# Optimization experiments

Measured on AMD Instinct MI355X. Metric: run time of the kernel, lower is better.

## Reference

```python
import jax, jax.numpy as jnp
import numpy as np
import math

B, T, C, E, H = 16, 256, 6, 512, 8


def setup_inputs() -> dict:
    key = jax.random.key(0)
    ks = jax.random.split(key, 5)
    std = 0.02
    return {
        "x": jax.random.normal(ks[0], (B, T, C, E), dtype=jnp.float32),
        "Wq": jax.random.normal(ks[1], (E, E), dtype=jnp.float32) * std,
        "bq": jnp.zeros((E,), dtype=jnp.float32),
        "Wk": jax.random.normal(ks[2], (E, E), dtype=jnp.float32) * std,
        "bk": jnp.zeros((E,), dtype=jnp.float32),
        "Wv": jax.random.normal(ks[3], (E, E), dtype=jnp.float32) * std,
        "bv": jnp.zeros((E,), dtype=jnp.float32),
        "Wp": jax.random.normal(ks[4], (E, E), dtype=jnp.float32) * std,
        "bp": jnp.zeros((E,), dtype=jnp.float32),
    }


def reference(x, Wq, bq, Wk, bk, Wv, bv, Wp, bp):
    b, t, c, e = x.shape
    hd = e // H
    # nn.Linear: y = x @ W^T + b, then view(B,T,C,H,hd).transpose(1,3) -> (B,H,C,T,hd)
    def heads(W, bias):
        y = jnp.einsum('btce,fe->btcf', x, W) + bias
        return y.reshape(b, t, c, H, hd).transpose(0, 3, 2, 1, 4)  # B,H,C,T,hd

    q = heads(Wq, bq)
    k = heads(Wk, bk)
    v = heads(Wv, bv)

    scale = 1.0 / math.sqrt(hd)
    att = jnp.einsum('bhctd,bhcsd->bhcts', q, k) * scale  # B,H,C,T,T
    causal = jnp.tril(jnp.ones((t, t), dtype=bool))
    att = jnp.where(causal, att, -jnp.inf)
    att = jax.nn.softmax(att, axis=-1)

    y = jnp.einsum('bhcts,bhcsd->bhctd', att, v)  # B,H,C,T,hd
    # permute(0,3,1,2,4) -> (B,T,H,C,hd), then view(B,T,C,E) (faithful to torch)
    y = y.transpose(0, 3, 1, 2, 4).reshape(b, t, c, e)
    return jnp.einsum('btce,fe->btcf', y, Wp) + bp
```

## Files before the change

kernel.cpp:

```cpp
#include <hip/hip_runtime.h>


typedef unsigned short u16;
typedef short bf16x8 __attribute__((ext_vector_type(8)));
typedef float f32x4 __attribute__((ext_vector_type(4)));
typedef u16 u16x4 __attribute__((ext_vector_type(4)));

#define MFMA16(a, b, c) __builtin_amdgcn_mfma_f32_16x16x32_bf16((a), (b), (c), 0, 0, 0)

__device__ __forceinline__ u16 f2b(float f) {
  union { float f; unsigned u; } v; v.f = f;
  unsigned r = v.u + 0x7fffu + ((v.u >> 16) & 1u);
  return (u16)(r >> 16);
}
__device__ __forceinline__ void gl_lds16(const void* g, void* l) {
  __builtin_amdgcn_global_load_lds(
      (const __attribute__((address_space(1))) void*)g,
      (__attribute__((address_space(3))) void*)l, 16, 0, 0);
}

__global__ void cvt_w(const float* W0, const float* W1, const float* W2,
                      const float* W3, u16* dst) {
  const float* src = (blockIdx.y == 0) ? W0 : (blockIdx.y == 1) ? W1
                   : (blockIdx.y == 2) ? W2 : W3;
  const int idx = (blockIdx.x * 256 + threadIdx.x) * 4;
  f32x4 v = *(const f32x4*)(src + idx);
  u16x4 o; o.x = f2b(v.x); o.y = f2b(v.y); o.z = f2b(v.z); o.w = f2b(v.w);
  *(u16x4*)(dst + (size_t)blockIdx.y * 262144 + idx) = o;
}

__global__ void cvt_x(const float* __restrict__ src, u16* __restrict__ dst) {
  const size_t idx = ((size_t)blockIdx.x * 256 + threadIdx.x) * 4;
  f32x4 v = *(const f32x4*)(src + idx);
  u16x4 o; o.x = f2b(v.x); o.y = f2b(v.y); o.z = f2b(v.z); o.w = f2b(v.w);
  *(u16x4*)(dst + idx) = o;
}

__global__ __launch_bounds__(256, 3) void gemm_bt(
    const u16* __restrict__ A,
    const u16* W0, const u16* W1, const u16* W2,
    const float* bs0, const float* bs1, const float* bs2,
    u16* O0, u16* O1, u16* O2,
    float* OF,
    int qkv_mode)
{
  const int z = blockIdx.z;
  const u16* W    = (z == 0) ? W0 : (z == 1) ? W1 : W2;
  const float* bs = (z == 0) ? bs0 : (z == 1) ? bs1 : bs2;
  u16* O          = (z == 0) ? O0 : (z == 1) ? O1 : O2;

  const int m0 = blockIdx.x * 128;
  const int n0 = blockIdx.y * 128;

  __shared__ u16 As[128 * 32];
  __shared__ u16 Bs[128 * 32];

  const int tid  = threadIdx.x;
  const int lane = tid & 63;
  const int wv   = tid >> 6;
  const int r    = lane & 15;
  const int qd   = lane >> 4;
  const int wm   = (wv & 1) * 64;
  const int wn   = (wv >> 1) * 64;

  f32x4 acc[4][4] = {};

  for (int k0 = 0; k0 < 512; k0 += 32) {
    __syncthreads();
    #pragma unroll
    for (int it = 0; it < 2; ++it) {
      const int flat = (it * 256 + tid) * 16;
      const int row  = flat >> 6;
      const int swc  = (flat >> 4) & 3;
      const int gc   = (swc - (row >> 1)) & 3;
      gl_lds16((const char*)A + (size_t)(m0 + row) * 1024 + k0 * 2 + gc * 16,
               (char*)As + flat);
      gl_lds16((const char*)W + (size_t)(n0 + row) * 1024 + k0 * 2 + gc * 16,
               (char*)Bs + flat);
    }
    __syncthreads();

    bf16x8 af[4], bf[4];
    #pragma unroll
    for (int mt = 0; mt < 4; ++mt) {
      const int row = wm + mt * 16 + r;
      const int sw  = (qd + (row >> 1)) & 3;
      af[mt] = *(const bf16x8*)((const char*)As + row * 64 + sw * 16);
    }
    #pragma unroll
    for (int nt = 0; nt < 4; ++nt) {
      const int row = wn + nt * 16 + r;
      const int sw  = (qd + (row >> 1)) & 3;
      bf[nt] = *(const bf16x8*)((const char*)Bs + row * 64 + sw * 16);
    }
    #pragma unroll
    for (int mt = 0; mt < 4; ++mt)
      #pragma unroll
      for (int nt = 0; nt < 4; ++nt)
        acc[mt][nt] = MFMA16(af[mt], bf[nt], acc[mt][nt]);
  }

  float bv[4];
  #pragma unroll
  for (int nt = 0; nt < 4; ++nt) bv[nt] = bs[n0 + wn + nt * 16 + r];

  if (qkv_mode) {
    #pragma unroll
    for (int mt = 0; mt < 4; ++mt) {
      #pragma unroll
      for (int rr = 0; rr < 4; ++rr) {
        const int m   = m0 + wm + mt * 16 + qd * 4 + rr;
        const int b   = m / 1536;
        const int rem = m - b * 1536;
        const int t   = rem / 6;
        const int c   = rem - t * 6;
        #pragma unroll
        for (int nt = 0; nt < 4; ++nt) {
          const int f = n0 + wn + nt * 16 + r;
          const int h = f >> 6;
          const int d = f & 63;
          const size_t addr = ((((size_t)b * 8 + h) * 6 + c) * 256 + t) * 64 + d;
          O[addr] = f2b(acc[mt][nt][rr] + bv[nt]);
        }
      }
    }
  } else {
    #pragma unroll
    for (int mt = 0; mt < 4; ++mt) {
      #pragma unroll
      for (int rr = 0; rr < 4; ++rr) {
        const int m = m0 + wm + mt * 16 + qd * 4 + rr;
        #pragma unroll
        for (int nt = 0; nt < 4; ++nt) {
          const int f = n0 + wn + nt * 16 + r;
          OF[(size_t)m * 512 + f] = acc[mt][nt][rr] + bv[nt];
        }
      }
    }
  }
}

__global__ __launch_bounds__(512, 2) void attn(
    const u16* __restrict__ q_ws, const u16* __restrict__ k_ws,
    const u16* __restrict__ v_ws, u16* __restrict__ y_ws)
{
  const int blk = blockIdx.x;
  const int b   = blk / 48;
  const int h   = (blk / 6) % 8;
  const int c   = blk % 6;
  const size_t base = (size_t)blk * 256 * 64;

  __shared__ u16 Ks[128 * 72];
  __shared__ u16 Vts[64 * 136];
  __shared__ u16 Ps[8][16 * 72];

  const int tid  = threadIdx.x;
  const int lane = tid & 63;
  const int wv   = tid >> 6;
  const int r    = lane & 15;
  const int qd   = lane >> 4;

  const int tiles[2] = { wv, 15 - wv };

  bf16x8 qf[2][2];
  #pragma unroll
  for (int ti = 0; ti < 2; ++ti)
    #pragma unroll
    for (int kc = 0; kc < 2; ++kc)
      qf[ti][kc] = *(const bf16x8*)(q_ws + base +
                     (size_t)(tiles[ti] * 16 + r) * 64 + kc * 32 + qd * 8);

  f32x4 o_acc[2][4] = {};
  float l_acc[2][4] = {{0.f,0.f,0.f,0.f},{0.f,0.f,0.f,0.f}};

  for (int sc = 0; sc < 2; ++sc) {
    __syncthreads();
    #pragma unroll
    for (int it = 0; it < 2; ++it) {
      const int idx = it * 512 + tid;
      const int row = idx >> 3;
      const int c8  = idx & 7;
      *(bf16x8*)(Ks + row * 72 + c8 * 8) =
          *(const bf16x8*)(k_ws + base + (size_t)(sc * 128 + row) * 64 + c8 * 8);
    }
    {
      const int jl = tid & 127;
      const int d0 = (tid >> 7) * 16;
      #pragma unroll
      for (int dd = 0; dd < 16; dd += 8) {
        bf16x8 vv = *(const bf16x8*)(v_ws + base +
                       (size_t)(sc * 128 + jl) * 64 + d0 + dd);
        #pragma unroll
        for (int e = 0; e < 8; ++e)
          Vts[(d0 + dd + e) * 136 + jl] = ((u16*)&vv)[e];
      }
    }
    __syncthreads();

    #pragma unroll
    for (int ti = 0; ti < 2; ++ti) {
      const int mt  = tiles[ti];
      const int i0  = mt * 16;
      const int nch = (mt >> 2) + 1;
      #pragma unroll
      for (int jcl = 0; jcl < 2; ++jcl) {
        const int jc = sc * 2 + jcl;
        if (jc >= nch) continue;
        const int j0l = jcl * 64;
        const int j0g = sc * 128 + j0l;

        f32x4 s[4] = {};
        #pragma unroll
        for (int nt = 0; nt < 4; ++nt)
          #pragma unroll
          for (int kc = 0; kc < 2; ++kc) {
            bf16x8 kf = *(const bf16x8*)(Ks + (j0l + nt * 16 + r) * 72 +
                                         kc * 32 + qd * 8);
            s[nt] = MFMA16(qf[ti][kc], kf, s[nt]);
          }

        #pragma unroll
        for (int nt = 0; nt < 4; ++nt)
          #pragma unroll
          for (int rr = 0; rr < 4; ++rr) {
            const int i = i0 + qd * 4 + rr;
            const int j = j0g + nt * 16 + r;
            float p = __builtin_exp2f(fminf(s[nt][rr], 500.f) *
                                      0.1803368801111244f);
            if (j > i) p = 0.f;
            l_acc[ti][rr] += p;
            Ps[wv][(qd * 4 + rr) * 72 + nt * 16 + r] = f2b(p);
          }
        asm volatile("s_waitcnt lgkmcnt(0)" ::: "memory");

        bf16x8 pf[2];
        #pragma unroll
        for (int kc = 0; kc < 2; ++kc)
          pf[kc] = *(const bf16x8*)(Ps[wv] + r * 72 + kc * 32 + qd * 8);
        #pragma unroll
        for (int ntd = 0; ntd < 4; ++ntd)
          #pragma unroll
          for (int kc = 0; kc < 2; ++kc) {
            bf16x8 vf = *(const bf16x8*)(Vts + (ntd * 16 + r) * 136 +
                                         j0l + kc * 32 + qd * 8);
            o_acc[ti][ntd] = MFMA16(pf[kc], vf, o_acc[ti][ntd]);
          }
      }
    }
  }

  const size_t obase = ((size_t)b * 256) * 3072 + h * 384 + c * 64;
  #pragma unroll
  for (int ti = 0; ti < 2; ++ti) {
    const int i0 = tiles[ti] * 16;
    float linv[4];
    #pragma unroll
    for (int rr = 0; rr < 4; ++rr) {
      float sum = l_acc[ti][rr];
      sum += __shfl_xor(sum, 1, 16);
      sum += __shfl_xor(sum, 2, 16);
      sum += __shfl_xor(sum, 4, 16);
      sum += __shfl_xor(sum, 8, 16);
      linv[rr] = 1.f / sum;
    }
    #pragma unroll
    for (int ntd = 0; ntd < 4; ++ntd)
      #pragma unroll
      for (int rr = 0; rr < 4; ++rr) {
        const int t = i0 + qd * 4 + rr;
        const int d = ntd * 16 + r;
        y_ws[obase + (size_t)t * 3072 + d] = f2b(o_acc[ti][ntd][rr] * linv[rr]);
      }
  }
}

extern "C" void kernel_launch(void* const* d_in, const int* in_sizes, int n_in,
                              void* d_out, int out_size, void* d_ws, size_t ws_size,
                              hipStream_t stream) {
  const float* x  = (const float*)d_in[0];
  const float* Wq = (const float*)d_in[1];
  const float* bq = (const float*)d_in[2];
  const float* Wk = (const float*)d_in[3];
  const float* bk = (const float*)d_in[4];
  const float* Wv = (const float*)d_in[5];
  const float* bv = (const float*)d_in[6];
  const float* Wp = (const float*)d_in[7];
  const float* bp = (const float*)d_in[8];
  float* out = (float*)d_out;

  const size_t PER_B = 256 * 6 * 512;
  const size_t WSEG  = 4 * 262144;

  int NB = 16;
  while (NB > 1 && (WSEG + (size_t)5 * NB * PER_B) * 2 > ws_size) NB >>= 1;

  u16* wbf = (u16*)d_ws;
  u16* Wqb = wbf;
  u16* Wkb = wbf + 262144;
  u16* Wvb = wbf + 2 * 262144;
  u16* Wpb = wbf + 3 * 262144;

  const size_t slab = (size_t)NB * PER_B;
  u16* xbf  = wbf + WSEG;
  u16* q_ws = xbf + slab;
  u16* k_ws = q_ws + slab;
  u16* v_ws = k_ws + slab;
  u16* y_ws = v_ws + slab;

  cvt_w<<<dim3(256, 4), 256, 0, stream>>>(Wq, Wk, Wv, Wp, wbf);

  const int nslab = 16 / NB;
  for (int s = 0; s < nslab; ++s) {
    const float* x_s  = x   + (size_t)s * NB * PER_B;
    float*      out_s = out + (size_t)s * NB * PER_B;
    cvt_x<<<dim3(NB * 768), 256, 0, stream>>>(x_s, xbf);
    gemm_bt<<<dim3(NB * 12, 4, 3), 256, 0, stream>>>(
        xbf, Wqb, Wkb, Wvb, bq, bk, bv, q_ws, k_ws, v_ws, nullptr, 1);
    attn<<<dim3(NB * 48), 512, 0, stream>>>(q_ws, k_ws, v_ws, y_ws);
    gemm_bt<<<dim3(NB * 12, 4, 1), 256, 0, stream>>>(
        y_ws, Wpb, Wpb, Wpb, bp, bp, bp, nullptr, nullptr, nullptr, out_s, 0);
  }
}
```

Baseline: 222.4 us.

## Fuse QKV projection into the attention kernel per batch-head-channel block

Replaces the separate QKV GEMM and attention kernels with one kernel. For each (b,h,c) it computes that head's Q, K and V slices from bf16 x and the weights, using a double-buffered global-to-LDS pipeline with swizzled layout, then runs causal attention directly from LDS. This removes the round trip of Q/K/V through global workspace and one kernel launch, and shrinks the workspace requirement. In exchange, each x tile is re-read once per head. The larger LDS footprint likely limits occupancy to one block per CU.

```diff
diff --git a/kernel.cpp b/kernel.cpp
--- a/kernel.cpp
+++ b/kernel.cpp
@@ -34,6 +34,209 @@
   f32x4 v = *(const f32x4*)(src + idx);
   u16x4 o; o.x = f2b(v.x); o.y = f2b(v.y); o.z = f2b(v.z); o.w = f2b(v.w);
   *(u16x4*)(dst + idx) = o;
+}
+
+#define STAGE(k, bi) do { \
+  _Pragma("unroll") \
+  for (int j_ = 0; j_ < 4; ++j_) \
+    if (j_ < 3 || tid < 256) \
+      gl_lds16(gsrc[j_] + (k) * 64, (char*)Ss[bi] + fl[j_]); \
+} while (0)
+
+__global__ __launch_bounds__(512, 2) void qkv_attn(
+    const u16* __restrict__ xbf, const u16* __restrict__ wbf,
+    const float* __restrict__ bq, const float* __restrict__ bk,
+    const float* __restrict__ bv, u16* __restrict__ y_ws)
+{
+  const int blk = blockIdx.x;
+  const int b   = blk / 48;
+  const int h   = (blk / 6) % 8;
+  const int c   = blk % 6;
+
+  __shared__ u16 Ss[2][448 * 32];
+  __shared__ u16 Ks[256 * 72];
+  __shared__ u16 Vts[64 * 264];
+  __shared__ u16 Qs[8][16 * 72];
+
+  const int tid  = threadIdx.x;
+  const int lane = tid & 63;
+  const int wv   = tid >> 6;
+  const int r    = lane & 15;
+  const int qd   = lane >> 4;
+  const int tiles[2] = { wv, 15 - wv };
+
+  const char* gsrc[4]; int fl[4];
+  #pragma unroll
+  for (int j = 0; j < 4; ++j) {
+    const int idx  = j * 512 + tid;
+    const int flat = idx * 16;
+    const int row  = flat >> 6;
+    const int gc   = (((flat >> 4) & 3) - (row >> 1)) & 3;
+    fl[j] = flat;
+    if (row < 256) {
+      gsrc[j] = (const char*)xbf +
+                ((size_t)(b * 256 + row) * 6 + c) * 1024 + gc * 16;
+    } else {
+      const int wr  = row - 256;
+      const int tau = (wr >> 6) & 3;
+      const int n   = wr & 63;
+      gsrc[j] = (const char*)wbf + (size_t)tau * 524288 +
+                (size_t)(h * 64 + n) * 1024 + gc * 16;
+    }
+  }
+
+  int aoff[2], boff[3][4];
+  #pragma unroll
+  for (int ti = 0; ti < 2; ++ti) {
+    const int row = tiles[ti] * 16 + r;
+    aoff[ti] = row * 64 + ((qd + (row >> 1)) & 3) * 16;
+  }
+  #pragma unroll
+  for (int tau = 0; tau < 3; ++tau)
+    #pragma unroll
+    for (int nt = 0; nt < 4; ++nt) {
+      const int row = 256 + tau * 64 + nt * 16 + r;
+      boff[tau][nt] = row * 64 + ((qd + (row >> 1)) & 3) * 16;
+    }
+
+  f32x4 acc[3][2][4] = {};
+
+  STAGE(0, 0);
+  __syncthreads();
+
+  #pragma unroll 2
+  for (int kt = 0; kt < 16; ++kt) {
+    const int bi = kt & 1;
+    if (kt < 15) STAGE(kt + 1, bi ^ 1);
+
+    bf16x8 af[2], bfr[3][4];
+    #pragma unroll
+    for (int ti = 0; ti < 2; ++ti)
+      af[ti] = *(const bf16x8*)((const char*)Ss[bi] + aoff[ti]);
+    #pragma unroll
+    for (int tau = 0; tau < 3; ++tau)
+      #pragma unroll
+      for (int nt = 0; nt < 4; ++nt)
+        bfr[tau][nt] = *(const bf16x8*)((const char*)Ss[bi] + boff[tau][nt]);
+
+    #pragma unroll
+    for (int tau = 0; tau < 3; ++tau)
+      #pragma unroll
+      for (int ti = 0; ti < 2; ++ti)
+        #pragma unroll
+        for (int nt = 0; nt < 4; ++nt)
+          acc[tau][ti][nt] = MFMA16(af[ti], bfr[tau][nt], acc[tau][ti][nt]);
+
+    __syncthreads();
+  }
+
+  float bqv[4], bkv[4], bvv[4];
+  #pragma unroll
+  for (int nt = 0; nt < 4; ++nt) {
+    const int col = h * 64 + nt * 16 + r;
+    bqv[nt] = bq[col]; bkv[nt] = bk[col]; bvv[nt] = bv[col];
+  }
+  #pragma unroll
+  for (int ti = 0; ti < 2; ++ti)
+    #pragma unroll
+    for (int nt = 0; nt < 4; ++nt)
+      #pragma unroll
+      for (int rr = 0; rr < 4; ++rr) {
+        const int trow = tiles[ti] * 16 + qd * 4 + rr;
+        const int col  = nt * 16 + r;
+        Ks[trow * 72 + col]  = f2b(acc[1][ti][nt][rr] + bkv[nt]);
+        Vts[col * 264 + trow] = f2b(acc[2][ti][nt][rr] + bvv[nt]);
+      }
+  __syncthreads();
+
+  f32x4 o_acc[2][4] = {};
+  float l_acc[2][4] = {{0.f,0.f,0.f,0.f},{0.f,0.f,0.f,0.f}};
+
+  #pragma unroll
+  for (int ti = 0; ti < 2; ++ti) {
+    const int mt  = tiles[ti];
+    const int i0  = mt * 16;
+    const int nch = (mt >> 2) + 1;
+
+    #pragma unroll
+    for (int nt = 0; nt < 4; ++nt)
+      #pragma unroll
+      for (int rr = 0; rr < 4; ++rr)
+        Qs[wv][(qd * 4 + rr) * 72 + nt * 16 + r] =
+            f2b(acc[0][ti][nt][rr] + bqv[nt]);
+    asm volatile("s_waitcnt lgkmcnt(0)" ::: "memory");
+
+    bf16x8 qf[2];
+    #pragma unroll
+    for (int kc = 0; kc < 2; ++kc)
+      qf[kc] = *(const bf16x8*)(Qs[wv] + r * 72 + kc * 32 + qd * 8);
+    asm volatile("s_waitcnt lgkmcnt(0)" ::: "memory");
+
+    for (int jc = 0; jc < nch; ++jc) {
+      const int j0 = jc * 64;
+
+      f32x4 s[4] = {};
+      #pragma unroll
+      for (int nt = 0; nt < 4; ++nt)
+        #pragma unroll
+        for (int kc = 0; kc < 2; ++kc) {
+          bf16x8 kf = *(const bf16x8*)(Ks + (j0 + nt * 16 + r) * 72 +
+                                       kc * 32 + qd * 8);
+          s[nt] = MFMA16(qf[kc], kf, s[nt]);
+        }
+
+      #pragma unroll
+      for (int nt = 0; nt < 4; ++nt)
+        #pragma unroll
+        for (int rr = 0; rr < 4; ++rr) {
+          const int i = i0 + qd * 4 + rr;
+          const int j = j0 + nt * 16 + r;
+          float p = __builtin_exp2f(fminf(s[nt][rr], 500.f) *
+                                    0.1803368801111244f);
+          if (j > i) p = 0.f;
+          l_acc[ti][rr] += p;
+          Qs[wv][(qd * 4 + rr) * 72 + nt * 16 + r] = f2b(p);
+        }
+      asm volatile("s_waitcnt lgkmcnt(0)" ::: "memory");
+
+      bf16x8 pf[2];
+      #pragma unroll
+      for (int kc = 0; kc < 2; ++kc)
+        pf[kc] = *(const bf16x8*)(Qs[wv] + r * 72 + kc * 32 + qd * 8);
+      #pragma unroll
+      for (int ntd = 0; ntd < 4; ++ntd)
+        #pragma unroll
+        for (int kc = 0; kc < 2; ++kc) {
+          bf16x8 vf = *(const bf16x8*)(Vts + (ntd * 16 + r) * 264 +
+                                       j0 + kc * 32 + qd * 8);
+          o_acc[ti][ntd] = MFMA16(pf[kc], vf, o_acc[ti][ntd]);
+        }
+    }
+  }
+
+  const size_t obase = ((size_t)b * 256) * 3072 + h * 384 + c * 64;
+  #pragma unroll
+  for (int ti = 0; ti < 2; ++ti) {
+    const int i0 = tiles[ti] * 16;
+    float linv[4];
+    #pragma unroll
+    for (int rr = 0; rr < 4; ++rr) {
+      float sum = l_acc[ti][rr];
+      sum += __shfl_xor(sum, 1, 16);
+      sum += __shfl_xor(sum, 2, 16);
+      sum += __shfl_xor(sum, 4, 16);
+      sum += __shfl_xor(sum, 8, 16);
+      linv[rr] = 1.f / sum;
+    }
+    #pragma unroll
+    for (int ntd = 0; ntd < 4; ++ntd)
+      #pragma unroll
+      for (int rr = 0; rr < 4; ++rr) {
+        const int t = i0 + qd * 4 + rr;
+        const int d = ntd * 16 + r;
+        y_ws[obase + (size_t)t * 3072 + d] = f2b(o_acc[ti][ntd][rr] * linv[rr]);
+      }
+  }
 }
 
 __global__ __launch_bounds__(256, 3) void gemm_bt(
@@ -117,9 +320,9 @@
         #pragma unroll
         for (int nt = 0; nt < 4; ++nt) {
           const int f = n0 + wn + nt * 16 + r;
-          const int h = f >> 6;
+          const int hh = f >> 6;
           const int d = f & 63;
-          const size_t addr = ((((size_t)b * 8 + h) * 6 + c) * 256 + t) * 64 + d;
+          const size_t addr = ((((size_t)b * 8 + hh) * 6 + c) * 256 + t) * 64 + d;
           O[addr] = f2b(acc[mt][nt][rr] + bv[nt]);
         }
       }
@@ -137,140 +340,6 @@
         }
       }
     }
-  }
-}
-
-__global__ __launch_bounds__(512, 2) void attn(
-    const u16* __restrict__ q_ws, const u16* __restrict__ k_ws,
-    const u16* __restrict__ v_ws, u16* __restrict__ y_ws)
-{
-  const int blk = blockIdx.x;
-  const int b   = blk / 48;
-  const int h   = (blk / 6) % 8;
-  const int c   = blk % 6;
-  const size_t base = (size_t)blk * 256 * 64;
-
-  __shared__ u16 Ks[128 * 72];
-  __shared__ u16 Vts[64 * 136];
-  __shared__ u16 Ps[8][16 * 72];
-
-  const int tid  = threadIdx.x;
-  const int lane = tid & 63;
-  const int wv   = tid >> 6;
-  const int r    = lane & 15;
-  const int qd   = lane >> 4;
-
-  const int tiles[2] = { wv, 15 - wv };
-
-  bf16x8 qf[2][2];
-  #pragma unroll
-  for (int ti = 0; ti < 2; ++ti)
-    #pragma unroll
-    for (int kc = 0; kc < 2; ++kc)
-      qf[ti][kc] = *(const bf16x8*)(q_ws + base +
-                     (size_t)(tiles[ti] * 16 + r) * 64 + kc * 32 + qd * 8);
-
-  f32x4 o_acc[2][4] = {};
-  float l_acc[2][4] = {{0.f,0.f,0.f,0.f},{0.f,0.f,0.f,0.f}};
-
-  for (int sc = 0; sc < 2; ++sc) {
-    __syncthreads();
-    #pragma unroll
-    for (int it = 0; it < 2; ++it) {
-      const int idx = it * 512 + tid;
-      const int row = idx >> 3;
-      const int c8  = idx & 7;
-      *(bf16x8*)(Ks + row * 72 + c8 * 8) =
-          *(const bf16x8*)(k_ws + base + (size_t)(sc * 128 + row) * 64 + c8 * 8);
-    }
-    {
-      const int jl = tid & 127;
-      const int d0 = (tid >> 7) * 16;
-      #pragma unroll
-      for (int dd = 0; dd < 16; dd += 8) {
-        bf16x8 vv = *(const bf16x8*)(v_ws + base +
-                       (size_t)(sc * 128 + jl) * 64 + d0 + dd);
-        #pragma unroll
-        for (int e = 0; e < 8; ++e)
-          Vts[(d0 + dd + e) * 136 + jl] = ((u16*)&vv)[e];
-      }
-    }
-    __syncthreads();
-
-    #pragma unroll
-    for (int ti = 0; ti < 2; ++ti) {
-      const int mt  = tiles[ti];
-      const int i0  = mt * 16;
-      const int nch = (mt >> 2) + 1;
-      #pragma unroll
-      for (int jcl = 0; jcl < 2; ++jcl) {
-        const int jc = sc * 2 + jcl;
-        if (jc >= nch) continue;
-        const int j0l = jcl * 64;
-        const int j0g = sc * 128 + j0l;
-
-        f32x4 s[4] = {};
-        #pragma unroll
-        for (int nt = 0; nt < 4; ++nt)
-          #pragma unroll
-          for (int kc = 0; kc < 2; ++kc) {
-            bf16x8 kf = *(const bf16x8*)(Ks + (j0l + nt * 16 + r) * 72 +
-                                         kc * 32 + qd * 8);
-            s[nt] = MFMA16(qf[ti][kc], kf, s[nt]);
-          }
-
-        #pragma unroll
-        for (int nt = 0; nt < 4; ++nt)
-          #pragma unroll
-          for (int rr = 0; rr < 4; ++rr) {
-            const int i = i0 + qd * 4 + rr;
-            const int j = j0g + nt * 16 + r;
-            float p = __builtin_exp2f(fminf(s[nt][rr], 500.f) *
-                                      0.1803368801111244f);
-            if (j > i) p = 0.f;
-            l_acc[ti][rr] += p;
-            Ps[wv][(qd * 4 + rr) * 72 + nt * 16 + r] = f2b(p);
-          }
-        asm volatile("s_waitcnt lgkmcnt(0)" ::: "memory");
-
-        bf16x8 pf[2];
-        #pragma unroll
-        for (int kc = 0; kc < 2; ++kc)
-          pf[kc] = *(const bf16x8*)(Ps[wv] + r * 72 + kc * 32 + qd * 8);
-        #pragma unroll
-        for (int ntd = 0; ntd < 4; ++ntd)
-          #pragma unroll
-          for (int kc = 0; kc < 2; ++kc) {
-            bf16x8 vf = *(const bf16x8*)(Vts + (ntd * 16 + r) * 136 +
-                                         j0l + kc * 32 + qd * 8);
-            o_acc[ti][ntd] = MFMA16(pf[kc], vf, o_acc[ti][ntd]);
-          }
-      }
-    }
-  }
-
-  const size_t obase = ((size_t)b * 256) * 3072 + h * 384 + c * 64;
-  #pragma unroll
-  for (int ti = 0; ti < 2; ++ti) {
-    const int i0 = tiles[ti] * 16;
-    float linv[4];
-    #pragma unroll
-    for (int rr = 0; rr < 4; ++rr) {
-      float sum = l_acc[ti][rr];
-      sum += __shfl_xor(sum, 1, 16);
-      sum += __shfl_xor(sum, 2, 16);
-      sum += __shfl_xor(sum, 4, 16);
-      sum += __shfl_xor(sum, 8, 16);
-      linv[rr] = 1.f / sum;
-    }
-    #pragma unroll
-    for (int ntd = 0; ntd < 4; ++ntd)
-      #pragma unroll
-      for (int rr = 0; rr < 4; ++rr) {
-        const int t = i0 + qd * 4 + rr;
-        const int d = ntd * 16 + r;
-        y_ws[obase + (size_t)t * 3072 + d] = f2b(o_acc[ti][ntd][rr] * linv[rr]);
-      }
   }
 }
 
@@ -292,20 +361,14 @@
   const size_t WSEG  = 4 * 262144;
 
   int NB = 16;
-  while (NB > 1 && (WSEG + (size_t)5 * NB * PER_B) * 2 > ws_size) NB >>= 1;
+  while (NB > 1 && (WSEG + (size_t)2 * NB * PER_B) * 2 > ws_size) NB >>= 1;
 
   u16* wbf = (u16*)d_ws;
-  u16* Wqb = wbf;
-  u16* Wkb = wbf + 262144;
-  u16* Wvb = wbf + 2 * 262144;
   u16* Wpb = wbf + 3 * 262144;
 
   const size_t slab = (size_t)NB * PER_B;
   u16* xbf  = wbf + WSEG;
-  u16* q_ws = xbf + slab;
-  u16* k_ws = q_ws + slab;
-  u16* v_ws = k_ws + slab;
-  u16* y_ws = v_ws + slab;
+  u16* y_ws = xbf + slab;
 
   cvt_w<<<dim3(256, 4), 256, 0, stream>>>(Wq, Wk, Wv, Wp, wbf);
 
@@ -314,9 +377,7 @@
     const float* x_s  = x   + (size_t)s * NB * PER_B;
     float*      out_s = out + (size_t)s * NB * PER_B;
     cvt_x<<<dim3(NB * 768), 256, 0, stream>>>(x_s, xbf);
-    gemm_bt<<<dim3(NB * 12, 4, 3), 256, 0, stream>>>(
-        xbf, Wqb, Wkb, Wvb, bq, bk, bv, q_ws, k_ws, v_ws, nullptr, 1);
-    attn<<<dim3(NB * 48), 512, 0, stream>>>(q_ws, k_ws, v_ws, y_ws);
+    qkv_attn<<<dim3(NB * 48), 512, 0, stream>>>(xbf, wbf, bq, bk, bv, y_ws);
     gemm_bt<<<dim3(NB * 12, 4, 1), 256, 0, stream>>>(
         y_ws, Wpb, Wpb, Wpb, bp, bp, bp, nullptr, nullptr, nullptr, out_s, 0);
   }
```

After: 202.1 us. 1.1x faster.
